# Kernel optimization log

Hardware: AMD Instinct MI355X
Metric: run time of the kernel (lower is better)

Reference implementation:

```python
import jax, jax.numpy as jnp
import numpy as np

N_EMBD = 1024
N_HEAD = 16
HEAD_DIM = N_EMBD // N_HEAD
SCALE = HEAD_DIM ** -0.5


def setup_inputs() -> dict:
    key = jax.random.key(0)
    ks = jax.random.split(key, 6)
    B, T = 64, 256
    s = N_EMBD ** -0.5
    return {
        "x": jax.random.normal(ks[0], (B, T, N_EMBD), dtype=jnp.float32),
        "Wq": jax.random.normal(ks[1], (N_EMBD, N_EMBD), dtype=jnp.float32) * s,
        "Wk": jax.random.normal(ks[2], (N_EMBD, N_EMBD), dtype=jnp.float32) * s,
        "Wv": jax.random.normal(ks[3], (N_EMBD, N_EMBD), dtype=jnp.float32) * s,
        "Wo": jax.random.normal(ks[4], (N_EMBD, N_EMBD), dtype=jnp.float32) * s,
        "bo": jax.random.normal(ks[5], (N_EMBD,), dtype=jnp.float32) * 0.01,
    }


def reference(x, Wq, Wk, Wv, Wo, bo):
    B, T, C = x.shape
    # QKV projections (no bias), split heads -> [B, H, T, Dh]
    def heads(y):
        return y.reshape(B, T, N_HEAD, HEAD_DIM).transpose(0, 2, 1, 3)
    q = heads(x @ Wq)
    k = heads(x @ Wk)
    v = heads(x @ Wv)
    # scaled causal attention scores [B, H, T, T]
    wei = jnp.einsum("bhqd,bhkd->bhqk", q, k) * SCALE
    causal = jnp.tril(jnp.ones((T, T), dtype=bool))
    wei = jnp.where(causal, wei, -jnp.inf)
    wei = jax.nn.softmax(wei, axis=-1)
    # dropout is identity in eval mode
    out = jnp.einsum("bhqk,bhkd->bhqd", wei, v)
    out = out.transpose(0, 2, 1, 3).reshape(B, T, C)
    return out @ Wo + bo
```

## Files before the change

### kernel.cpp

```cpp
#include <hip/hip_runtime.h>
#include <hip/hip_bf16.h>
#include <stdint.h>

typedef __attribute__((ext_vector_type(8))) short bfx8;
typedef __attribute__((ext_vector_type(4))) short bfx4;
typedef __attribute__((ext_vector_type(4))) float f32x4;
typedef __attribute__((ext_vector_type(4))) unsigned short us4;

#define SCALE_ATT 0.125f

__device__ __forceinline__ unsigned short f2bf(float f) {
  union { float f; unsigned u; } a; a.f = f;
  unsigned r = a.u + 0x7fffu + ((a.u >> 16) & 1u);
  return (unsigned short)(r >> 16);
}

__device__ __forceinline__ void gll16(const void* g, void* l) {
  __builtin_amdgcn_global_load_lds(
      (__attribute__((address_space(1))) void*)(g),
      (__attribute__((address_space(3))) void*)(l), 16, 0, 0);
}

__device__ __forceinline__ bfx8 ld2x64(const unsigned short* p) {
  bfx4 lo = *(const bfx4*)p;
  bfx4 hi = *(const bfx4*)(p + 4);
  return __builtin_shufflevector(lo, hi, 0, 1, 2, 3, 4, 5, 6, 7);
}

__global__ __launch_bounds__(256) void cvt_x(const float* __restrict__ x,
                                             unsigned short* __restrict__ xb, int n4) {
  int i = blockIdx.x * blockDim.x + threadIdx.x;
  int stride = gridDim.x * blockDim.x;
  const float4* x4 = (const float4*)x;
  for (; i < n4; i += stride) {
    float4 v = x4[i];
    us4 o;
    o[0] = f2bf(v.x); o[1] = f2bf(v.y); o[2] = f2bf(v.z); o[3] = f2bf(v.w);
    *(us4*)&xb[(size_t)i * 4] = o;
  }
}

__global__ __launch_bounds__(256) void cvt_w(const float* __restrict__ W0, const float* __restrict__ W1,
                                             const float* __restrict__ W2, const float* __restrict__ W3,
                                             unsigned short* __restrict__ T0, unsigned short* __restrict__ T1,
                                             unsigned short* __restrict__ T2, unsigned short* __restrict__ T3) {
  const float* W; unsigned short* T;
  switch (blockIdx.z) {
    case 0: W = W0; T = T0; break;
    case 1: W = W1; T = T1; break;
    case 2: W = W2; T = T2; break;
    default: W = W3; T = T3; break;
  }
  __shared__ unsigned short Ts[64][68];
  int k0 = blockIdx.x * 64, n0 = blockIdx.y * 64;
  int t = threadIdx.x;
  int lrow = t >> 4, c4 = t & 15;
  #pragma unroll
  for (int i = 0; i < 4; i++) {
    int row = lrow + i * 16;
    float4 v = *(const float4*)&W[(size_t)(k0 + row) * 1024 + n0 + c4 * 4];
    Ts[c4 * 4 + 0][row] = f2bf(v.x);
    Ts[c4 * 4 + 1][row] = f2bf(v.y);
    Ts[c4 * 4 + 2][row] = f2bf(v.z);
    Ts[c4 * 4 + 3][row] = f2bf(v.w);
  }
  __syncthreads();
  #pragma unroll
  for (int i = 0; i < 4; i++) {
    int nrow = lrow + i * 16;
    us4 v = *(const us4*)&Ts[nrow][c4 * 4];
    *(us4*)&T[(size_t)(n0 + nrow) * 1024 + k0 + c4 * 4] = v;
  }
}

#define DS_BAR() __builtin_amdgcn_s_barrier()
#define SB0() __builtin_amdgcn_sched_barrier(0)
#define LGKM(N) do { asm volatile("s_waitcnt lgkmcnt(" #N ")" ::: "memory"); \
                     __builtin_amdgcn_sched_barrier(0); } while (0)
#define VMW4() asm volatile("s_waitcnt vmcnt(4)" ::: "memory")
#define VMW0() asm volatile("s_waitcnt vmcnt(0)" ::: "memory")

#define STAGE(hs, gb, r0, kbyte) do { \
  const char* _g = (const char*)(gb) + (size_t)((r0) + srow) * 2048 + (size_t)(kbyte) + scolb; \
  gll16(_g, (hs) + w * 1024); \
  gll16(_g + 16 * 2048, (hs) + w * 1024 + 512); \
} while (0)

#define LOADA(dst, ptr, qm) \
  _Pragma("unroll") for (int mi = 0; mi < 4; ++mi) \
    dst[mi] = *(const bfx8*)&(ptr)[(wm * 128 + (qm) * 64 + mi * 16 + lr) * 32 + rcol];

#define LOADB(dst, ptr) \
  _Pragma("unroll") for (int ni = 0; ni < 4; ++ni) \
    dst[ni] = *(const bfx8*)&(ptr)[(wn * 64 + ni * 16 + lr) * 32 + rcol];

#define MFMA16(rb, a, b) \
  _Pragma("unroll") for (int mi = 0; mi < 4; ++mi) \
    _Pragma("unroll") for (int ni = 0; ni < 4; ++ni) \
      acc[(rb) + mi][ni] = __builtin_amdgcn_mfma_f32_16x16x32_bf16(a[mi], b[ni], acc[(rb) + mi][ni], 0, 0, 0);

#define HALF(Ac, Bc, bfr, An, Bn, KB, STG) do {                               \
    LOADA(af, Ac, 0);                                                         \
    LOADB(bfr, Bc);                                                           \
    SB0();                                                                    \
    LOADA(ag, Ac, 1);                                                         \
    SB0();                                                                    \
    if (STG) { STAGE(An, A, am0, KB); STAGE(Bn, Bt, n0, KB); SB0(); }         \
    LGKM(4);                                                                  \
    __builtin_amdgcn_s_setprio(1);  MFMA16(0, af, bfr);                       \
    __builtin_amdgcn_s_setprio(0);                                            \
    LGKM(0);                                                                  \
    __builtin_amdgcn_s_setprio(1);  MFMA16(4, ag, bfr);                       \
    __builtin_amdgcn_s_setprio(0);                                            \
  } while (0)

template<int MODE>
__global__ __launch_bounds__(512, 2) void gemm8p(
    const unsigned short* __restrict__ A,
    const unsigned short* __restrict__ Bt0, const unsigned short* __restrict__ Bt1,
    const unsigned short* __restrict__ Bt2,
    unsigned short* __restrict__ O0, unsigned short* __restrict__ O1,
    unsigned short* __restrict__ O2,
    const float* __restrict__ bias, float* __restrict__ OutF, int nby) {
  __shared__ unsigned short A0s[2][256 * 32];
  __shared__ unsigned short B0s[2][256 * 32];
  __shared__ unsigned short A1s[2][256 * 32];
  __shared__ unsigned short B1s[2][256 * 32];

  int tid = threadIdx.x;
  int w = tid >> 6, l = tid & 63;
  int lr = l & 15, lh = l >> 4;
  int wm = w >> 2, wn = w & 3;
  int srow = w * 32 + (l >> 2);
  int scolb = ((l & 3) * 16) ^ (((l >> 5) & 1) << 5);
  int rcol = (lh * 8) ^ (((lr >> 3) & 1) << 4);

  int cpx = gridDim.x >> 3;
  int o = blockIdx.x;
  int wg = (o & 7) * cpx + (o >> 3);
  int bm = wg / nby, bn = wg % nby;

  const unsigned short* Bt;
  unsigned short* Ob = nullptr;
  int n0;
  if (MODE == 0) {
    int sel = bn >> 2;
    n0 = (bn & 3) * 256;
    Bt = sel == 0 ? Bt0 : (sel == 1 ? Bt1 : Bt2);
    Ob = sel == 0 ? O0 : (sel == 1 ? O1 : O2);
  } else {
    Bt = Bt0;
    n0 = bn * 256;
  }
  int am0 = bm * 256;

  f32x4 acc[8][4];
  #pragma unroll
  for (int i = 0; i < 8; ++i)
    #pragma unroll
    for (int jj = 0; jj < 4; ++jj) acc[i][jj] = (f32x4){0.f, 0.f, 0.f, 0.f};

  bfx8 af[4], ag[4], bf0[4], bf1[4];

  STAGE(A0s[0], A, am0, 0);   SB0();
  STAGE(B0s[0], Bt, n0, 0);   SB0();
  STAGE(A1s[0], A, am0, 64);  SB0();
  STAGE(B1s[0], Bt, n0, 64);  SB0();
  VMW4();
  DS_BAR();

  int cur = 0;
  #pragma unroll 1
  for (int t = 0; t < 15; ++t) {
    int kb = (t + 1) * 128;
    unsigned short* A0c = A0s[cur];       unsigned short* B0c = B0s[cur];
    unsigned short* A1c = A1s[cur];       unsigned short* B1c = B1s[cur];
    unsigned short* A0n = A0s[cur ^ 1];   unsigned short* B0n = B0s[cur ^ 1];
    unsigned short* A1n = A1s[cur ^ 1];   unsigned short* B1n = B1s[cur ^ 1];
    HALF(A0c, B0c, bf0, A0n, B0n, kb, 1);
    VMW4();
    DS_BAR();
    HALF(A1c, B1c, bf1, A1n, B1n, kb + 64, 1);
    VMW4();
    DS_BAR();
    cur ^= 1;
  }
  HALF(A0s[1], B0s[1], bf0, (unsigned short*)0, (unsigned short*)0, 0, 0);
  VMW0();
  DS_BAR();
  HALF(A1s[1], B1s[1], bf1, (unsigned short*)0, (unsigned short*)0, 0, 0);

  float bv[4];
  if (MODE == 1) {
    #pragma unroll
    for (int ni = 0; ni < 4; ++ni) bv[ni] = bias[n0 + wn * 64 + ni * 16 + lr];
  }
  #pragma unroll
  for (int mi8 = 0; mi8 < 8; ++mi8)
    #pragma unroll
    for (int ni = 0; ni < 4; ++ni)
      #pragma unroll
      for (int j = 0; j < 4; ++j) {
        int r = am0 + wm * 128 + mi8 * 16 + lh * 4 + j;
        int c = n0 + wn * 64 + ni * 16 + lr;
        if (MODE == 0)
          Ob[(size_t)r * 1024 + c] = f2bf(acc[mi8][ni][j]);
        else
          OutF[(size_t)r * 1024 + c] = acc[mi8][ni][j] + bv[ni];
      }
}

__global__ __launch_bounds__(256, 4) void attn_kernel(
    const unsigned short* __restrict__ Qb, const unsigned short* __restrict__ Kb,
    const unsigned short* __restrict__ Vb, unsigned short* __restrict__ Ab) {
  __shared__ unsigned short Vt[64][260];
  __shared__ unsigned short Pw[4][16][36];

  int t = threadIdx.x;
  int w = t >> 6, l = t & 63;
  int lr = l & 15, lh = l >> 4;
  int bh = blockIdx.x;
  size_t rowbase = (size_t)(bh >> 4) * 256 * 1024 + (size_t)(bh & 15) * 64;

  {
    int rr = t >> 3, part = t & 7;
    for (int i = 0; i < 8; i++) {
      int row = i * 32 + rr;
      bfx8 vv = *(const bfx8*)(Vb + rowbase + (size_t)row * 1024 + part * 8);
      #pragma unroll
      for (int e = 0; e < 8; e++) Vt[part * 8 + e][row] = (unsigned short)vv[e];
    }
  }
  __syncthreads();

  for (int qt = 0; qt < 4; qt++) {
    int r0 = qt * 64 + w * 16;
    int rmax = r0 + 15;
    const unsigned short* Qrow = Qb + rowbase + (size_t)(r0 + lr) * 1024 + lh * 8;
    bfx8 aq0 = *(const bfx8*)(Qrow);
    bfx8 aq1 = *(const bfx8*)(Qrow + 32);

    float m[4], lsum[4];
    #pragma unroll
    for (int j = 0; j < 4; j++) { m[j] = -1e30f; lsum[j] = 0.f; }
    f32x4 oc[4];
    #pragma unroll
    for (int ct = 0; ct < 4; ct++) oc[ct] = (f32x4){0.f, 0.f, 0.f, 0.f};

    int nkc = (rmax >> 6) + 1;
    for (int kc = 0; kc < nkc; kc++) {
      int kbase = kc * 64;
      bool haveB = (kbase + 32) <= rmax;
      const unsigned short* Kr = Kb + rowbase + (size_t)(kbase + lr) * 1024 + lh * 8;

      bfx8 k0a = *(const bfx8*)(Kr);
      bfx8 k0b = *(const bfx8*)(Kr + 32);
      bfx8 k1a = *(const bfx8*)(Kr + 16 * 1024);
      bfx8 k1b = *(const bfx8*)(Kr + 16 * 1024 + 32);
      f32x4 s0 = (f32x4){0.f, 0.f, 0.f, 0.f};
      f32x4 s1 = (f32x4){0.f, 0.f, 0.f, 0.f};
      f32x4 s2 = (f32x4){0.f, 0.f, 0.f, 0.f};
      f32x4 s3 = (f32x4){0.f, 0.f, 0.f, 0.f};
      s0 = __builtin_amdgcn_mfma_f32_16x16x32_bf16(aq0, k0a, s0, 0, 0, 0);
      s0 = __builtin_amdgcn_mfma_f32_16x16x32_bf16(aq1, k0b, s0, 0, 0, 0);
      s1 = __builtin_amdgcn_mfma_f32_16x16x32_bf16(aq0, k1a, s1, 0, 0, 0);
      s1 = __builtin_amdgcn_mfma_f32_16x16x32_bf16(aq1, k1b, s1, 0, 0, 0);
      if (haveB) {
        bfx8 k2a = *(const bfx8*)(Kr + 32 * 1024);
        bfx8 k2b = *(const bfx8*)(Kr + 32 * 1024 + 32);
        bfx8 k3a = *(const bfx8*)(Kr + 48 * 1024);
        bfx8 k3b = *(const bfx8*)(Kr + 48 * 1024 + 32);
        s2 = __builtin_amdgcn_mfma_f32_16x16x32_bf16(aq0, k2a, s2, 0, 0, 0);
        s2 = __builtin_amdgcn_mfma_f32_16x16x32_bf16(aq1, k2b, s2, 0, 0, 0);
        s3 = __builtin_amdgcn_mfma_f32_16x16x32_bf16(aq0, k3a, s3, 0, 0, 0);
        s3 = __builtin_amdgcn_mfma_f32_16x16x32_bf16(aq1, k3b, s3, 0, 0, 0);
      }

      int c0 = kbase + lr, c1 = c0 + 16, c2 = c0 + 32, c3 = c0 + 48;
      unsigned pb[4];
      #pragma unroll
      for (int j = 0; j < 4; j++) {
        int row = r0 + lh * 4 + j;
        float v0 = (c0 <= row) ? s0[j] : -1e30f;
        float v1 = (c1 <= row) ? s1[j] : -1e30f;
        float v2 = (c2 <= row) ? s2[j] : -1e30f;
        float v3 = (c3 <= row) ? s3[j] : -1e30f;
        float cm = fmaxf(fmaxf(v0, v1), fmaxf(v2, v3));
        cm = fmaxf(cm, __shfl_xor(cm, 1));
        cm = fmaxf(cm, __shfl_xor(cm, 2));
        cm = fmaxf(cm, __shfl_xor(cm, 4));
        cm = fmaxf(cm, __shfl_xor(cm, 8));
        float mn = fmaxf(m[j], cm);
        float sc = __expf((m[j] - mn) * SCALE_ATT);
        float p0 = (c0 <= row) ? __expf((s0[j] - mn) * SCALE_ATT) : 0.f;
        float p1 = (c1 <= row) ? __expf((s1[j] - mn) * SCALE_ATT) : 0.f;
        float p2 = (c2 <= row) ? __expf((s2[j] - mn) * SCALE_ATT) : 0.f;
        float p3 = (c3 <= row) ? __expf((s3[j] - mn) * SCALE_ATT) : 0.f;
        m[j] = mn;
        float cs = (p0 + p1) + (p2 + p3);
        cs += __shfl_xor(cs, 1);
        cs += __shfl_xor(cs, 2);
        cs += __shfl_xor(cs, 4);
        cs += __shfl_xor(cs, 8);
        lsum[j] = lsum[j] * sc + cs;
        #pragma unroll
        for (int ct = 0; ct < 4; ct++) oc[ct][j] *= sc;
        Pw[w][lh * 4 + j][lr] = f2bf(p0);
        Pw[w][lh * 4 + j][16 + lr] = f2bf(p1);
        pb[j] = (unsigned)f2bf(p2) | ((unsigned)f2bf(p3) << 16);
      }

      {
        bfx8 pa = ld2x64(&Pw[w][lr][lh * 8]);
        #pragma unroll
        for (int ct = 0; ct < 4; ct++) {
          bfx8 vb = ld2x64(&Vt[ct * 16 + lr][kbase + lh * 8]);
          oc[ct] = __builtin_amdgcn_mfma_f32_16x16x32_bf16(pa, vb, oc[ct], 0, 0, 0);
        }
      }
      if (haveB) {
        #pragma unroll
        for (int j = 0; j < 4; j++) {
          Pw[w][lh * 4 + j][lr] = (unsigned short)(pb[j] & 0xffffu);
          Pw[w][lh * 4 + j][16 + lr] = (unsigned short)(pb[j] >> 16);
        }
        bfx8 pa = ld2x64(&Pw[w][lr][lh * 8]);
        #pragma unroll
        for (int ct = 0; ct < 4; ct++) {
          bfx8 vb = ld2x64(&Vt[ct * 16 + lr][kbase + 32 + lh * 8]);
          oc[ct] = __builtin_amdgcn_mfma_f32_16x16x32_bf16(pa, vb, oc[ct], 0, 0, 0);
        }
      }
    }

    float rinv[4];
    #pragma unroll
    for (int j = 0; j < 4; j++) rinv[j] = 1.0f / lsum[j];
    #pragma unroll
    for (int ct = 0; ct < 4; ct++)
      #pragma unroll
      for (int j = 0; j < 4; j++) {
        int row = r0 + lh * 4 + j;
        Ab[rowbase + (size_t)row * 1024 + ct * 16 + lr] = f2bf(oc[ct][j] * rinv[j]);
      }
  }
}

extern "C" void kernel_launch(void* const* d_in, const int* in_sizes, int n_in,
                              void* d_out, int out_size, void* d_ws, size_t ws_size,
                              hipStream_t stream) {
  const float* x  = (const float*)d_in[0];
  const float* Wq = (const float*)d_in[1];
  const float* Wk = (const float*)d_in[2];
  const float* Wv = (const float*)d_in[3];
  const float* Wo = (const float*)d_in[4];
  const float* bo = (const float*)d_in[5];
  float* out = (float*)d_out;

  char* ws = (char*)d_ws;
  unsigned short* xb  = (unsigned short*)(ws);
  unsigned short* Wtq = (unsigned short*)(ws + (size_t)(32u << 20));
  unsigned short* Wtk = (unsigned short*)(ws + (size_t)(34u << 20));
  unsigned short* Wtv = (unsigned short*)(ws + (size_t)(36u << 20));
  unsigned short* Wto = (unsigned short*)(ws + (size_t)(38u << 20));
  unsigned short* Qb  = (unsigned short*)(ws + (size_t)(40u << 20));
  unsigned short* Kb  = (unsigned short*)(ws + (size_t)(72u << 20));
  unsigned short* Vb  = (unsigned short*)(ws + (size_t)(104u << 20));
  unsigned short* Ab  = xb;

  cvt_x<<<2048, 256, 0, stream>>>(x, xb, 4194304);
  cvt_w<<<dim3(16, 16, 4), 256, 0, stream>>>(Wq, Wk, Wv, Wo, Wtq, Wtk, Wtv, Wto);
  gemm8p<0><<<768, 512, 0, stream>>>(xb, Wtq, Wtk, Wtv, Qb, Kb, Vb, nullptr, nullptr, 12);
  attn_kernel<<<1024, 256, 0, stream>>>(Qb, Kb, Vb, Ab);
  gemm8p<1><<<256, 512, 0, stream>>>(Ab, Wto, Wto, Wto, nullptr, nullptr, nullptr, bo, out, 4);
}
```

Baseline: 222.5 us.

## Pre-swizzle weight into MFMA fragment layout and load B directly from global

The weight transpose kernel now writes B in a fragment-tiled layout, 16-row by 32-k blocks of 512 elements, so each lane's bfx8 operand is contiguous. The GEMM drops the LDS staging for B and loads B fragments straight from global into registers one k-half ahead, keeping only A in shared memory. This halves LDS use and removes the B ds_reads and their bank traffic. In exchange it relies on global/L2 latency being hidden by the prefetch, with tightened vmcnt waits, and the main loop is restructured around this.

```diff
diff --git a/kernel.cpp b/kernel.cpp
--- a/kernel.cpp
+++ b/kernel.cpp
@@ -65,20 +65,25 @@
     Ts[c4 * 4 + 3][row] = f2bf(v.w);
   }
   __syncthreads();
+  int f = t >> 5, sub = t & 31;
+  int nt_l = f >> 1, ks_l = f & 1;
+  size_t base = ((size_t)(((n0 >> 4) + nt_l) * 32 + (k0 >> 5) + ks_l)) * 512;
   #pragma unroll
-  for (int i = 0; i < 4; i++) {
-    int nrow = lrow + i * 16;
-    us4 v = *(const us4*)&Ts[nrow][c4 * 4];
-    *(us4*)&T[(size_t)(n0 + nrow) * 1024 + k0 + c4 * 4] = v;
+  for (int i = 0; i < 2; i++) {
+    int l = sub * 2 + i;
+    int row = nt_l * 16 + (l & 15);
+    int col = ks_l * 32 + ((l >> 4) << 3);
+    us4 a = *(const us4*)&Ts[row][col];
+    us4 b = *(const us4*)&Ts[row][col + 4];
+    *(us4*)&T[base + l * 8] = a;
+    *(us4*)&T[base + l * 8 + 4] = b;
   }
 }
 
 #define DS_BAR() __builtin_amdgcn_s_barrier()
 #define SB0() __builtin_amdgcn_sched_barrier(0)
-#define LGKM(N) do { asm volatile("s_waitcnt lgkmcnt(" #N ")" ::: "memory"); \
-                     __builtin_amdgcn_sched_barrier(0); } while (0)
-#define VMW4() asm volatile("s_waitcnt vmcnt(4)" ::: "memory")
-#define VMW0() asm volatile("s_waitcnt vmcnt(0)" ::: "memory")
+#define LGKM(N) do { asm volatile("s_waitcnt lgkmcnt(" #N ")" ::: "memory"); SB0(); } while (0)
+#define VMW(N) do { asm volatile("s_waitcnt vmcnt(" #N ")" ::: "memory"); SB0(); } while (0)
 
 #define STAGE(hs, gb, r0, kbyte) do { \
   const char* _g = (const char*)(gb) + (size_t)((r0) + srow) * 2048 + (size_t)(kbyte) + scolb; \
@@ -90,29 +95,14 @@
   _Pragma("unroll") for (int mi = 0; mi < 4; ++mi) \
     dst[mi] = *(const bfx8*)&(ptr)[(wm * 128 + (qm) * 64 + mi * 16 + lr) * 32 + rcol];
 
-#define LOADB(dst, ptr) \
+#define LOADBG(dst, ks) \
   _Pragma("unroll") for (int ni = 0; ni < 4; ++ni) \
-    dst[ni] = *(const bfx8*)&(ptr)[(wn * 64 + ni * 16 + lr) * 32 + rcol];
+    dst[ni] = *(const bfx8*)&Bpw[((size_t)(ni * 32 + (ks))) * 512];
 
 #define MFMA16(rb, a, b) \
   _Pragma("unroll") for (int mi = 0; mi < 4; ++mi) \
     _Pragma("unroll") for (int ni = 0; ni < 4; ++ni) \
       acc[(rb) + mi][ni] = __builtin_amdgcn_mfma_f32_16x16x32_bf16(a[mi], b[ni], acc[(rb) + mi][ni], 0, 0, 0);
-
-#define HALF(Ac, Bc, bfr, An, Bn, KB, STG) do {                               \
-    LOADA(af, Ac, 0);                                                         \
-    LOADB(bfr, Bc);                                                           \
-    SB0();                                                                    \
-    LOADA(ag, Ac, 1);                                                         \
-    SB0();                                                                    \
-    if (STG) { STAGE(An, A, am0, KB); STAGE(Bn, Bt, n0, KB); SB0(); }         \
-    LGKM(4);                                                                  \
-    __builtin_amdgcn_s_setprio(1);  MFMA16(0, af, bfr);                       \
-    __builtin_amdgcn_s_setprio(0);                                            \
-    LGKM(0);                                                                  \
-    __builtin_amdgcn_s_setprio(1);  MFMA16(4, ag, bfr);                       \
-    __builtin_amdgcn_s_setprio(0);                                            \
-  } while (0)
 
 template<int MODE>
 __global__ __launch_bounds__(512, 2) void gemm8p(
@@ -123,9 +113,7 @@
     unsigned short* __restrict__ O2,
     const float* __restrict__ bias, float* __restrict__ OutF, int nby) {
   __shared__ unsigned short A0s[2][256 * 32];
-  __shared__ unsigned short B0s[2][256 * 32];
   __shared__ unsigned short A1s[2][256 * 32];
-  __shared__ unsigned short B1s[2][256 * 32];
 
   int tid = threadIdx.x;
   int w = tid >> 6, l = tid & 63;
@@ -153,6 +141,7 @@
     n0 = bn * 256;
   }
   int am0 = bm * 256;
+  const unsigned short* Bpw = Bt + ((size_t)((n0 >> 4) + wn * 4) * 32) * 512 + (size_t)l * 8;
 
   f32x4 acc[8][4];
   #pragma unroll
@@ -160,35 +149,56 @@
     #pragma unroll
     for (int jj = 0; jj < 4; ++jj) acc[i][jj] = (f32x4){0.f, 0.f, 0.f, 0.f};
 
-  bfx8 af[4], ag[4], bf0[4], bf1[4];
-
-  STAGE(A0s[0], A, am0, 0);   SB0();
-  STAGE(B0s[0], Bt, n0, 0);   SB0();
-  STAGE(A1s[0], A, am0, 64);  SB0();
-  STAGE(B1s[0], Bt, n0, 64);  SB0();
-  VMW4();
+  bfx8 af[4], ag[4], b0[4], b1[4];
+
+  STAGE(A0s[0], A, am0, 0);   STAGE(A1s[0], A, am0, 64);  SB0();
+  LOADBG(b0, 0); SB0();
+  LOADBG(b1, 1); SB0();
+  VMW(8);
   DS_BAR();
 
   int cur = 0;
   #pragma unroll 1
   for (int t = 0; t < 15; ++t) {
     int kb = (t + 1) * 128;
-    unsigned short* A0c = A0s[cur];       unsigned short* B0c = B0s[cur];
-    unsigned short* A1c = A1s[cur];       unsigned short* B1c = B1s[cur];
-    unsigned short* A0n = A0s[cur ^ 1];   unsigned short* B0n = B0s[cur ^ 1];
-    unsigned short* A1n = A1s[cur ^ 1];   unsigned short* B1n = B1s[cur ^ 1];
-    HALF(A0c, B0c, bf0, A0n, B0n, kb, 1);
-    VMW4();
-    DS_BAR();
-    HALF(A1c, B1c, bf1, A1n, B1n, kb + 64, 1);
-    VMW4();
+    int ks2 = (t + 1) * 2;
+    unsigned short* A0c = A0s[cur];       unsigned short* A1c = A1s[cur];
+    unsigned short* A0n = A0s[cur ^ 1];   unsigned short* A1n = A1s[cur ^ 1];
+    LOADA(af, A0c, 0);  LOADA(ag, A0c, 1);  SB0();
+    STAGE(A0n, A, am0, kb);  STAGE(A1n, A, am0, kb + 64);  SB0();
+    LGKM(4); VMW(8);
+    __builtin_amdgcn_s_setprio(1);  MFMA16(0, af, b0);
+    __builtin_amdgcn_s_setprio(0);
+    LGKM(0);
+    __builtin_amdgcn_s_setprio(1);  MFMA16(4, ag, b0);
+    __builtin_amdgcn_s_setprio(0);
+    LOADBG(b0, ks2); SB0();
+    LOADA(af, A1c, 0);  LOADA(ag, A1c, 1);  SB0();
+    LGKM(4); VMW(8);
+    __builtin_amdgcn_s_setprio(1);  MFMA16(0, af, b1);
+    __builtin_amdgcn_s_setprio(0);
+    LGKM(0);
+    __builtin_amdgcn_s_setprio(1);  MFMA16(4, ag, b1);
+    __builtin_amdgcn_s_setprio(0);
+    LOADBG(b1, ks2 + 1); SB0();
+    VMW(8);
     DS_BAR();
     cur ^= 1;
   }
-  HALF(A0s[1], B0s[1], bf0, (unsigned short*)0, (unsigned short*)0, 0, 0);
-  VMW0();
-  DS_BAR();
-  HALF(A1s[1], B1s[1], bf1, (unsigned short*)0, (unsigned short*)0, 0, 0);
+  LOADA(af, A0s[1], 0);  LOADA(ag, A0s[1], 1);  SB0();
+  LGKM(4); VMW(4);
+  __builtin_amdgcn_s_setprio(1);  MFMA16(0, af, b0);
+  __builtin_amdgcn_s_setprio(0);
+  LGKM(0);
+  __builtin_amdgcn_s_setprio(1);  MFMA16(4, ag, b0);
+  __builtin_amdgcn_s_setprio(0);
+  LOADA(af, A1s[1], 0);  LOADA(ag, A1s[1], 1);  SB0();
+  LGKM(4); VMW(0);
+  __builtin_amdgcn_s_setprio(1);  MFMA16(0, af, b1);
+  __builtin_amdgcn_s_setprio(0);
+  LGKM(0);
+  __builtin_amdgcn_s_setprio(1);  MFMA16(4, ag, b1);
+  __builtin_amdgcn_s_setprio(0);
 
   float bv[4];
   if (MODE == 1) {
```

Result: faster. 209.1 us (-6.0%).
